# Kernel optimization log

Measured on AMD Instinct MI355X. Metric: run time of the kernel, lower is better.

## Reference

```python
import jax, jax.numpy as jnp
import numpy as np

TEMP = 1.0
POOL_K = 0.5
BN_EPS = 1e-5
B, N, D = 16, 256, 128


def setup_inputs() -> dict:
    key = jax.random.key(0)
    ks = jax.random.split(key, 8)
    s = 0.05
    return {
        "x": jax.random.normal(ks[0], (B, N, D), jnp.float32),
        "att_proj_w": jax.random.normal(ks[1], (D, D), jnp.float32) * s,
        "att_proj_b": jnp.zeros((D,), jnp.float32),
        "att_weight": jax.random.normal(ks[2], (D, 1), jnp.float32) * s,
        "pwa_w": jax.random.normal(ks[3], (D, D), jnp.float32) * s,
        "pwa_b": jnp.zeros((D,), jnp.float32),
        "pwoa_w": jax.random.normal(ks[4], (D, D), jnp.float32) * s,
        "pwoa_b": jnp.zeros((D,), jnp.float32),
        "bn_gamma": jnp.ones((D,), jnp.float32),
        "bn_beta": jnp.zeros((D,), jnp.float32),
        "bn_mean": jnp.zeros((D,), jnp.float32),
        "bn_var": jnp.ones((D,), jnp.float32),
        "pool_w": jax.random.normal(ks[5], (D, 1), jnp.float32) * s,
        "pool_b": jnp.zeros((1,), jnp.float32),
    }


def reference(x, att_proj_w, att_proj_b, att_weight, pwa_w, pwa_b,
              pwoa_w, pwoa_b, bn_gamma, bn_beta, bn_mean, bn_var,
              pool_w, pool_b):
    # ---- GraphAttentionLayer (eval mode: dropout = identity) ----
    # pairwise node outer product: (B, N, N, D)
    pair = x[:, :, None, :] * x[:, None, :, :]
    # att_proj + tanh, then project to scalar per node pair
    a = jnp.tanh(pair @ att_proj_w + att_proj_b)          # (B,N,N,D)
    logits = (a @ att_weight)[..., 0] / TEMP              # (B,N,N)
    # softmax over dim=-2 (the first node axis of the (N,N) map)
    att = jax.nn.softmax(logits, axis=1)                  # (B,N,N)
    # project: att_map @ x through proj_with_att, plus skip branch
    agg = jnp.einsum("bij,bjd->bid", att, x)              # (B,N,D)
    h = (agg @ pwa_w + pwa_b) + (x @ pwoa_w + pwoa_b)
    # BatchNorm1d in eval mode over feature dim
    h = (h - bn_mean) * jax.lax.rsqrt(bn_var + BN_EPS) * bn_gamma + bn_beta
    h = jax.nn.selu(h)
    # ---- GraphPool (eval mode: dropout = identity) ----
    scores = jax.nn.sigmoid(h @ pool_w + pool_b)          # (B,N,1)
    k_nodes = max(int(N * POOL_K), 1)
    _, idx = jax.lax.top_k(scores[..., 0], k_nodes)       # (B,k)
    hs = h * scores                                       # (B,N,D)
    out = jnp.take_along_axis(hs, idx[:, :, None], axis=1)  # (B,k,D)
    return out
```

## Files before the change

### kernel.cpp

```cpp
#include <hip/hip_runtime.h>
#include <math.h>

typedef float f32x4 __attribute__((ext_vector_type(4)));
typedef short s16x8 __attribute__((ext_vector_type(8)));

#define L2E 1.4426950408889634f
#define C2L2E 2.885390081777927f

__global__ void k0_prep(const float* __restrict__ W,
                        unsigned short* __restrict__ gWhi,
                        unsigned short* __restrict__ gWlo) {
  int t = blockIdx.x * 256 + threadIdx.x;
  int d = t >> 7, e = t & 127;
  float w = W[d * 128 + e];
  unsigned u = __float_as_uint(w);
  unsigned hb = (u + 0x7fffu + ((u >> 16) & 1u)) >> 16;
  float r = w - __uint_as_float(hb << 16);
  unsigned ul = __float_as_uint(r);
  unsigned lb = (ul + 0x7fffu + ((ul >> 16) & 1u)) >> 16;
  int addr = e * 128 + (d ^ ((e & 7) << 3));
  gWhi[addr] = (unsigned short)hb;
  gWlo[addr] = (unsigned short)lb;
}

__global__ __launch_bounds__(256, 2) void k1_logits(
    const float* __restrict__ x, const unsigned short* __restrict__ gWhi,
    const unsigned short* __restrict__ gWlo, const float* __restrict__ apb,
    const float* __restrict__ av, float* __restrict__ Lg) {
  __shared__ __align__(16) unsigned short sWhi[16384];
  __shared__ __align__(16) unsigned short sWlo[16384];
  __shared__ __align__(16) float sXj[16 * 132];

  int tt = blockIdx.x, ti = 0;
  while (tt >= 16 - ti) { tt -= 16 - ti; ++ti; }
  const int tj = ti + tt;
  const int b = blockIdx.y;
  const int i0 = ti * 16, j0 = tj * 16;
  const int tid = threadIdx.x;

  {
    const uint4* shi = (const uint4*)gWhi;
    const uint4* slo = (const uint4*)gWlo;
    uint4* dhi = (uint4*)sWhi;
    uint4* dlo = (uint4*)sWlo;
#pragma unroll
    for (int r = 0; r < 8; ++r) {
      dhi[tid + 256 * r] = shi[tid + 256 * r];
      dlo[tid + 256 * r] = slo[tid + 256 * r];
    }
    const float4* xsrc = (const float4*)(x + ((size_t)(b * 256 + j0)) * 128);
#pragma unroll
    for (int r = 0; r < 2; ++r) {
      int v = tid + 256 * r;
      *(float4*)&sXj[(v >> 5) * 132 + (v & 31) * 4] = xsrc[v];
    }
  }
  __syncthreads();

  const int lane = tid & 63;
  const int w = tid >> 6;
  const int quad = lane >> 4;
  const int col = lane & 15;
  const int swz = (col & 7) << 3;

  float vw[8];
  f32x4 acc[4][8];
#pragma unroll
  for (int et = 0; et < 8; ++et) {
    float bi = apb[col + 16 * et];
    vw[et] = av[col + 16 * et];
#pragma unroll
    for (int mt = 0; mt < 4; ++mt) acc[mt][et] = (f32x4){bi, bi, bi, bi};
  }

  const float* xib = x + ((size_t)(b * 256 + i0 + 4 * w)) * 128;

#pragma unroll
  for (int kstep = 0; kstep < 4; ++kstep) {
    const int k0 = kstep * 32 + quad * 8;
    float4 xj0 = *(const float4*)&sXj[col * 132 + k0];
    float4 xj1 = *(const float4*)&sXj[col * 132 + k0 + 4];
    s16x8 Ah[4], Al[4];
#pragma unroll
    for (int mt = 0; mt < 4; ++mt) {
      const float* xip = xib + mt * 128 + k0;
      float4 xi0 = *(const float4*)xip;
      float4 xi1 = *(const float4*)(xip + 4);
      float pv[8];
      pv[0] = xi0.x * xj0.x; pv[1] = xi0.y * xj0.y;
      pv[2] = xi0.z * xj0.z; pv[3] = xi0.w * xj0.w;
      pv[4] = xi1.x * xj1.x; pv[5] = xi1.y * xj1.y;
      pv[6] = xi1.z * xj1.z; pv[7] = xi1.w * xj1.w;
      uint4 hp, lp;
      unsigned* hq = (unsigned*)&hp;
      unsigned* lq = (unsigned*)&lp;
#pragma unroll
      for (int p = 0; p < 4; ++p) {
        unsigned u0 = __float_as_uint(pv[2 * p]);
        unsigned u1 = __float_as_uint(pv[2 * p + 1]);
        hq[p] = __builtin_amdgcn_perm(u1, u0, 0x07060302);
        float h0 = __uint_as_float(u0 & 0xffff0000u);
        float h1 = __uint_as_float(u1 & 0xffff0000u);
        unsigned v0 = __float_as_uint(pv[2 * p] - h0) + 0x8000u;
        unsigned v1 = __float_as_uint(pv[2 * p + 1] - h1) + 0x8000u;
        lq[p] = __builtin_amdgcn_perm(v1, v0, 0x07060302);
      }
      Ah[mt] = *(s16x8*)&hp;
      Al[mt] = *(s16x8*)&lp;
    }
#pragma unroll
    for (int et = 0; et < 8; ++et) {
      const int addr = (col + 16 * et) * 128 + (k0 ^ swz);
      s16x8 bh = *(const s16x8*)&sWhi[addr];
      s16x8 bl = *(const s16x8*)&sWlo[addr];
#pragma unroll
      for (int mt = 0; mt < 4; ++mt) {
        acc[mt][et] = __builtin_amdgcn_mfma_f32_16x16x32_bf16(Ah[mt], bh, acc[mt][et], 0, 0, 0);
        acc[mt][et] = __builtin_amdgcn_mfma_f32_16x16x32_bf16(Al[mt], bh, acc[mt][et], 0, 0, 0);
        acc[mt][et] = __builtin_amdgcn_mfma_f32_16x16x32_bf16(Ah[mt], bl, acc[mt][et], 0, 0, 0);
      }
    }
  }

  float fl[4];
#pragma unroll
  for (int mt = 0; mt < 4; ++mt) {
    float ls[4] = {0.f, 0.f, 0.f, 0.f};
#pragma unroll
    for (int et = 0; et < 8; ++et) {
#pragma unroll
      for (int r = 0; r < 4; ++r) {
        float e2 = __builtin_amdgcn_exp2f(acc[mt][et][r] * C2L2E);
        float t = 1.0f - 2.0f * __builtin_amdgcn_rcpf(e2 + 1.0f);
        ls[r] += t * vw[et];
      }
    }
#pragma unroll
    for (int m = 1; m < 16; m <<= 1) {
      ls[0] += __shfl_xor(ls[0], m);
      ls[1] += __shfl_xor(ls[1], m);
      ls[2] += __shfl_xor(ls[2], m);
      ls[3] += __shfl_xor(ls[3], m);
    }
    fl[mt] = (col == 0) ? ls[0] : (col == 1) ? ls[1] : (col == 2) ? ls[2] : ls[3];
  }
  if (col < 4) {
    const int j = j0 + quad * 4 + col;
    float4 val = {fl[0], fl[1], fl[2], fl[3]};
    *(float4*)&Lg[((size_t)(b * 256 + j)) * 256 + i0 + 4 * w] = val;
    if (ti != tj) {
#pragma unroll
      for (int mt = 0; mt < 4; ++mt)
        Lg[((size_t)(b * 256 + i0 + 4 * w + mt)) * 256 + j] = fl[mt];
    }
  }
}

__global__ void k2_softmax(float* __restrict__ Lg) {
  const int w = threadIdx.x >> 6, lane = threadIdx.x & 63;
  const int row = blockIdx.x * 4 + w;
  float4* p = (float4*)(Lg + (size_t)row * 256);
  float4 v = p[lane];
  float m = fmaxf(fmaxf(v.x, v.y), fmaxf(v.z, v.w));
#pragma unroll
  for (int mask = 1; mask < 64; mask <<= 1) m = fmaxf(m, __shfl_xor(m, mask));
  v.x = __builtin_amdgcn_exp2f((v.x - m) * L2E);
  v.y = __builtin_amdgcn_exp2f((v.y - m) * L2E);
  v.z = __builtin_amdgcn_exp2f((v.z - m) * L2E);
  v.w = __builtin_amdgcn_exp2f((v.w - m) * L2E);
  float s = v.x + v.y + v.z + v.w;
#pragma unroll
  for (int mask = 1; mask < 64; mask <<= 1) s += __shfl_xor(s, mask);
  float inv = 1.0f / s;
  v.x *= inv; v.y *= inv; v.z *= inv; v.w *= inv;
  p[lane] = v;
}

__global__ void k34_aggh(const float* __restrict__ Lg, const float* __restrict__ x,
                         const float* __restrict__ pwa, const float* __restrict__ pwoa,
                         const float* __restrict__ pwab, const float* __restrict__ pwob,
                         const float* __restrict__ gam, const float* __restrict__ bet,
                         const float* __restrict__ mea, const float* __restrict__ varr,
                         float* __restrict__ h) {
  const int b = blockIdx.y, i0 = blockIdx.x * 8;
  const int tid = threadIdx.x;
  const int il = tid >> 5, dl = tid & 31;
  __shared__ float satt[16][8];
  __shared__ float sxj[2048];
  __shared__ float sa[1024];
  __shared__ float sxi[1024];

  ((float4*)sxi)[tid] = ((const float4*)(x + ((size_t)(b * 256 + i0)) * 128))[tid];

  float acc[4] = {0.f, 0.f, 0.f, 0.f};
  for (int jj = 0; jj < 256; jj += 16) {
    __syncthreads();
    if (tid < 128)
      satt[tid >> 3][tid & 7] =
          Lg[((size_t)(b * 256 + jj + (tid >> 3))) * 256 + i0 + (tid & 7)];
    const float4* xsrc = (const float4*)(x + ((size_t)(b * 256 + jj)) * 128);
    ((float4*)sxj)[tid] = xsrc[tid];
    ((float4*)sxj)[tid + 256] = xsrc[tid + 256];
    __syncthreads();
#pragma unroll
    for (int jl = 0; jl < 16; ++jl) {
      float a = satt[jl][il];
      float4 xv = *(const float4*)&sxj[jl * 128 + dl * 4];
      acc[0] += a * xv.x; acc[1] += a * xv.y;
      acc[2] += a * xv.z; acc[3] += a * xv.w;
    }
  }
  __syncthreads();
  *(float4*)&sa[il * 128 + dl * 4] = *(float4*)acc;
  __syncthreads();

  double z[4] = {0, 0, 0, 0};
  for (int k = 0; k < 128; ++k) {
    double a = (double)sa[il * 128 + k];
    float4 wv = *(const float4*)(pwa + k * 128 + dl * 4);
    z[0] += a * (double)wv.x; z[1] += a * (double)wv.y;
    z[2] += a * (double)wv.z; z[3] += a * (double)wv.w;
  }
  for (int k = 0; k < 128; ++k) {
    double a = (double)sxi[il * 128 + k];
    float4 wv = *(const float4*)(pwoa + k * 128 + dl * 4);
    z[0] += a * (double)wv.x; z[1] += a * (double)wv.y;
    z[2] += a * (double)wv.z; z[3] += a * (double)wv.w;
  }
  float* dst = h + ((size_t)(b * 256 + i0 + il)) * 128 + dl * 4;
  float o[4];
#pragma unroll
  for (int q = 0; q < 4; ++q) {
    int d = dl * 4 + q;
    double hv = z[q] + (double)pwab[d] + (double)pwob[d];
    double bn = (hv - (double)mea[d]) * (1.0 / sqrt((double)varr[d] + 1e-5)) *
                    (double)gam[d] +
                (double)bet[d];
    float bf = (float)bn;
    o[q] = bf > 0.f ? 1.0507009873554805f * bf
                    : 1.7580993408473766f *
                          (__builtin_amdgcn_exp2f(bf * L2E) - 1.0f);
  }
  *(float4*)dst = *(float4*)o;
}

__global__ __launch_bounds__(1024) void k5_topk(const float* __restrict__ h,
                                                const float* __restrict__ plw,
                                                const float* __restrict__ plb,
                                                float* __restrict__ out) {
  const int b = blockIdx.x, tid = threadIdx.x;
  const int t = tid >> 2, c = tid & 3;
  __shared__ double part[256][4];
  __shared__ int ipart[256][4];
  __shared__ float sc[256];
  __shared__ int sel[128];

  {
    const float* hr = h + ((size_t)(b * 256 + t)) * 128 + c * 32;
    const float* wr = plw + c * 32;
    double z = 0.0;
    for (int k = 0; k < 32; ++k) z += (double)hr[k] * (double)wr[k];
    part[t][c] = z;
  }
  __syncthreads();
  if (c == 0) {
    double zz = part[t][0] + part[t][1] + part[t][2] + part[t][3] + (double)plb[0];
    sc[t] = (float)(1.0 / (1.0 + exp(-zz)));
  }
  __syncthreads();
  {
    const float st = sc[t];
    int r = 0;
    for (int m = c * 64; m < c * 64 + 64; ++m) {
      float sm = sc[m];
      r += (sm > st) || (sm == st && m < t);
    }
    ipart[t][c] = r;
  }
  __syncthreads();
  if (c == 0) {
    int rank = ipart[t][0] + ipart[t][1] + ipart[t][2] + ipart[t][3];
    if (rank < 128) sel[rank] = t;
  }
  __syncthreads();
  const float4* h4 = (const float4*)(h + (size_t)b * 256 * 128);
  float4* o4 = (float4*)(out + (size_t)b * 128 * 128);
#pragma unroll
  for (int r = 0; r < 4; ++r) {
    int v = tid + 1024 * r;
    int row = v >> 5, q = v & 31;
    int src = sel[row];
    float ss = sc[src];
    float4 hv = h4[src * 32 + q];
    float4 ov;
    ov.x = hv.x * ss; ov.y = hv.y * ss; ov.z = hv.z * ss; ov.w = hv.w * ss;
    o4[row * 32 + q] = ov;
  }
}

extern "C" void kernel_launch(void* const* d_in, const int* in_sizes, int n_in,
                              void* d_out, int out_size, void* d_ws, size_t ws_size,
                              hipStream_t stream) {
  const float* x    = (const float*)d_in[0];
  const float* apw  = (const float*)d_in[1];
  const float* apb  = (const float*)d_in[2];
  const float* av   = (const float*)d_in[3];
  const float* pwa  = (const float*)d_in[4];
  const float* pwab = (const float*)d_in[5];
  const float* pwoa = (const float*)d_in[6];
  const float* pwob = (const float*)d_in[7];
  const float* gam  = (const float*)d_in[8];
  const float* bet  = (const float*)d_in[9];
  const float* mea  = (const float*)d_in[10];
  const float* varr = (const float*)d_in[11];
  const float* plw  = (const float*)d_in[12];
  const float* plb  = (const float*)d_in[13];
  float* out = (float*)d_out;

  unsigned short* gWhi = (unsigned short*)d_ws;
  unsigned short* gWlo = gWhi + 16384;
  float* Lg = (float*)((char*)d_ws + 65536);
  float* hb = Lg + (size_t)16 * 256 * 256;

  k0_prep<<<64, 256, 0, stream>>>(apw, gWhi, gWlo);
  k1_logits<<<dim3(136, 16), 256, 0, stream>>>(x, gWhi, gWlo, apb, av, Lg);
  k2_softmax<<<1024, 256, 0, stream>>>(Lg);
  k34_aggh<<<dim3(32, 16), 256, 0, stream>>>(Lg, x, pwa, pwoa, pwab, pwob, gam,
                                             bet, mea, varr, hb);
  k5_topk<<<16, 1024, 0, stream>>>(hb, plw, plb, out);
}
```

Before: 189.2 us.

## Fuse softmax into logits kernel via exp and atomic row sums; move pool scores

```diff
diff --git a/kernel.cpp b/kernel.cpp
--- a/kernel.cpp
+++ b/kernel.cpp
@@ -9,27 +9,36 @@
 
 __global__ void k0_prep(const float* __restrict__ W,
                         unsigned short* __restrict__ gWhi,
-                        unsigned short* __restrict__ gWlo) {
-  int t = blockIdx.x * 256 + threadIdx.x;
-  int d = t >> 7, e = t & 127;
-  float w = W[d * 128 + e];
-  unsigned u = __float_as_uint(w);
-  unsigned hb = (u + 0x7fffu + ((u >> 16) & 1u)) >> 16;
-  float r = w - __uint_as_float(hb << 16);
-  unsigned ul = __float_as_uint(r);
-  unsigned lb = (ul + 0x7fffu + ((ul >> 16) & 1u)) >> 16;
-  int addr = e * 128 + (d ^ ((e & 7) << 3));
-  gWhi[addr] = (unsigned short)hb;
-  gWlo[addr] = (unsigned short)lb;
-}
-
-__global__ __launch_bounds__(256, 2) void k1_logits(
+                        unsigned short* __restrict__ gWlo,
+                        float* __restrict__ S) {
+  int bid = blockIdx.x;
+  if (bid < 64) {
+    int t = bid * 256 + threadIdx.x;
+    int d = t >> 7, e = t & 127;
+    float w = W[d * 128 + e];
+    unsigned u = __float_as_uint(w);
+    unsigned hb = (u + 0x7fffu + ((u >> 16) & 1u)) >> 16;
+    float r = w - __uint_as_float(hb << 16);
+    unsigned ul = __float_as_uint(r);
+    unsigned lb = (ul + 0x7fffu + ((ul >> 16) & 1u)) >> 16;
+    int addr = e * 128 + (d ^ ((e & 7) << 3));
+    gWhi[addr] = (unsigned short)hb;
+    gWlo[addr] = (unsigned short)lb;
+  } else {
+    S[(bid - 64) * 256 + threadIdx.x] = 0.f;
+  }
+}
+
+__global__ __launch_bounds__(256, 2) void kA_logits(
     const float* __restrict__ x, const unsigned short* __restrict__ gWhi,
     const unsigned short* __restrict__ gWlo, const float* __restrict__ apb,
-    const float* __restrict__ av, float* __restrict__ Lg) {
+    const float* __restrict__ av, float* __restrict__ Lg,
+    float* __restrict__ S) {
   __shared__ __align__(16) unsigned short sWhi[16384];
   __shared__ __align__(16) unsigned short sWlo[16384];
   __shared__ __align__(16) float sXj[16 * 132];
+  __shared__ float sRow[16][4];
+  __shared__ float sMir[16];
 
   int tt = blockIdx.x, ti = 0;
   while (tt >= 16 - ti) { tt -= 16 - ti; ++ti; }
@@ -122,7 +131,7 @@
     }
   }
 
-  float fl[4];
+  float E[4];
 #pragma unroll
   for (int mt = 0; mt < 4; ++mt) {
     float ls[4] = {0.f, 0.f, 0.f, 0.f};
@@ -142,54 +151,59 @@
       ls[2] += __shfl_xor(ls[2], m);
       ls[3] += __shfl_xor(ls[3], m);
     }
-    fl[mt] = (col == 0) ? ls[0] : (col == 1) ? ls[1] : (col == 2) ? ls[2] : ls[3];
-  }
+    float fl = (col == 0) ? ls[0] : (col == 1) ? ls[1] : (col == 2) ? ls[2] : ls[3];
+    E[mt] = __builtin_amdgcn_exp2f(fl * L2E);
+  }
+
   if (col < 4) {
     const int j = j0 + quad * 4 + col;
-    float4 val = {fl[0], fl[1], fl[2], fl[3]};
+    float4 val = {E[0], E[1], E[2], E[3]};
     *(float4*)&Lg[((size_t)(b * 256 + j)) * 256 + i0 + 4 * w] = val;
-    if (ti != tj) {
+    sRow[quad * 4 + col][w] = E[0] + E[1] + E[2] + E[3];
+  }
+
+  if (ti != tj) {
+    if (col < 4) {
+      const int j = j0 + quad * 4 + col;
 #pragma unroll
       for (int mt = 0; mt < 4; ++mt)
-        Lg[((size_t)(b * 256 + i0 + 4 * w + mt)) * 256 + j] = fl[mt];
-    }
-  }
-}
-
-__global__ void k2_softmax(float* __restrict__ Lg) {
-  const int w = threadIdx.x >> 6, lane = threadIdx.x & 63;
-  const int row = blockIdx.x * 4 + w;
-  float4* p = (float4*)(Lg + (size_t)row * 256);
-  float4 v = p[lane];
-  float m = fmaxf(fmaxf(v.x, v.y), fmaxf(v.z, v.w));
-#pragma unroll
-  for (int mask = 1; mask < 64; mask <<= 1) m = fmaxf(m, __shfl_xor(m, mask));
-  v.x = __builtin_amdgcn_exp2f((v.x - m) * L2E);
-  v.y = __builtin_amdgcn_exp2f((v.y - m) * L2E);
-  v.z = __builtin_amdgcn_exp2f((v.z - m) * L2E);
-  v.w = __builtin_amdgcn_exp2f((v.w - m) * L2E);
-  float s = v.x + v.y + v.z + v.w;
-#pragma unroll
-  for (int mask = 1; mask < 64; mask <<= 1) s += __shfl_xor(s, mask);
-  float inv = 1.0f / s;
-  v.x *= inv; v.y *= inv; v.z *= inv; v.w *= inv;
-  p[lane] = v;
-}
-
-__global__ void k34_aggh(const float* __restrict__ Lg, const float* __restrict__ x,
-                         const float* __restrict__ pwa, const float* __restrict__ pwoa,
-                         const float* __restrict__ pwab, const float* __restrict__ pwob,
-                         const float* __restrict__ gam, const float* __restrict__ bet,
-                         const float* __restrict__ mea, const float* __restrict__ varr,
-                         float* __restrict__ h) {
+        Lg[((size_t)(b * 256 + i0 + 4 * w + mt)) * 256 + j] = E[mt];
+    }
+#pragma unroll
+    for (int mt = 0; mt < 4; ++mt) {
+      float v = (col < 4) ? E[mt] : 0.f;
+#pragma unroll
+      for (int m = 1; m < 64; m <<= 1) v += __shfl_xor(v, m);
+      if (lane == 0) sMir[4 * w + mt] = v;
+    }
+  }
+  __syncthreads();
+  if (tid < 16) {
+    atomicAdd(&S[b * 256 + j0 + tid],
+              sRow[tid][0] + sRow[tid][1] + sRow[tid][2] + sRow[tid][3]);
+    if (ti != tj) atomicAdd(&S[b * 256 + i0 + tid], sMir[tid]);
+  }
+}
+
+__global__ void kB_aggh(const float* __restrict__ Lg, const float* __restrict__ S,
+                        const float* __restrict__ x,
+                        const float* __restrict__ pwa, const float* __restrict__ pwoa,
+                        const float* __restrict__ pwab, const float* __restrict__ pwob,
+                        const float* __restrict__ gam, const float* __restrict__ bet,
+                        const float* __restrict__ mea, const float* __restrict__ varr,
+                        const float* __restrict__ plw, const float* __restrict__ plb,
+                        float* __restrict__ h, float* __restrict__ scores) {
   const int b = blockIdx.y, i0 = blockIdx.x * 8;
   const int tid = threadIdx.x;
   const int il = tid >> 5, dl = tid & 31;
+  __shared__ float sInv[256];
   __shared__ float satt[16][8];
   __shared__ float sxj[2048];
   __shared__ float sa[1024];
   __shared__ float sxi[1024];
-
+  __shared__ double sScD[8][32];
+
+  sInv[tid] = 1.0f / S[b * 256 + tid];
   ((float4*)sxi)[tid] = ((const float4*)(x + ((size_t)(b * 256 + i0)) * 128))[tid];
 
   float acc[4] = {0.f, 0.f, 0.f, 0.f};
@@ -197,7 +211,8 @@
     __syncthreads();
     if (tid < 128)
       satt[tid >> 3][tid & 7] =
-          Lg[((size_t)(b * 256 + jj + (tid >> 3))) * 256 + i0 + (tid & 7)];
+          Lg[((size_t)(b * 256 + jj + (tid >> 3))) * 256 + i0 + (tid & 7)] *
+          sInv[jj + (tid >> 3)];
     const float4* xsrc = (const float4*)(x + ((size_t)(b * 256 + jj)) * 128);
     ((float4*)sxj)[tid] = xsrc[tid];
     ((float4*)sxj)[tid + 256] = xsrc[tid + 256];
@@ -227,7 +242,6 @@
     z[0] += a * (double)wv.x; z[1] += a * (double)wv.y;
     z[2] += a * (double)wv.z; z[3] += a * (double)wv.w;
   }
-  float* dst = h + ((size_t)(b * 256 + i0 + il)) * 128 + dl * 4;
   float o[4];
 #pragma unroll
   for (int q = 0; q < 4; ++q) {
@@ -241,32 +255,30 @@
                     : 1.7580993408473766f *
                           (__builtin_amdgcn_exp2f(bf * L2E) - 1.0f);
   }
-  *(float4*)dst = *(float4*)o;
-}
-
-__global__ __launch_bounds__(1024) void k5_topk(const float* __restrict__ h,
-                                                const float* __restrict__ plw,
-                                                const float* __restrict__ plb,
+  *(float4*)(h + ((size_t)(b * 256 + i0 + il)) * 128 + dl * 4) = *(float4*)o;
+
+  sScD[il][dl] = (double)o[0] * (double)plw[dl * 4] +
+                 (double)o[1] * (double)plw[dl * 4 + 1] +
+                 (double)o[2] * (double)plw[dl * 4 + 2] +
+                 (double)o[3] * (double)plw[dl * 4 + 3];
+  __syncthreads();
+  if (tid < 8) {
+    double zz = (double)plb[0];
+    for (int c = 0; c < 32; ++c) zz += sScD[tid][c];
+    scores[b * 256 + i0 + tid] = (float)(1.0 / (1.0 + exp(-zz)));
+  }
+}
+
+__global__ __launch_bounds__(1024) void kC_topk(const float* __restrict__ h,
+                                                const float* __restrict__ scores,
                                                 float* __restrict__ out) {
   const int b = blockIdx.x, tid = threadIdx.x;
   const int t = tid >> 2, c = tid & 3;
-  __shared__ double part[256][4];
+  __shared__ float sc[256];
   __shared__ int ipart[256][4];
-  __shared__ float sc[256];
   __shared__ int sel[128];
 
-  {
-    const float* hr = h + ((size_t)(b * 256 + t)) * 128 + c * 32;
-    const float* wr = plw + c * 32;
-    double z = 0.0;
-    for (int k = 0; k < 32; ++k) z += (double)hr[k] * (double)wr[k];
-    part[t][c] = z;
-  }
-  __syncthreads();
-  if (c == 0) {
-    double zz = part[t][0] + part[t][1] + part[t][2] + part[t][3] + (double)plb[0];
-    sc[t] = (float)(1.0 / (1.0 + exp(-zz)));
-  }
+  if (c == 0) sc[t] = scores[b * 256 + t];
   __syncthreads();
   {
     const float st = sc[t];
@@ -319,13 +331,14 @@
 
   unsigned short* gWhi = (unsigned short*)d_ws;
   unsigned short* gWlo = gWhi + 16384;
-  float* Lg = (float*)((char*)d_ws + 65536);
+  float* S  = (float*)((char*)d_ws + 65536);
+  float* Lg = (float*)((char*)d_ws + 81920);
   float* hb = Lg + (size_t)16 * 256 * 256;
-
-  k0_prep<<<64, 256, 0, stream>>>(apw, gWhi, gWlo);
-  k1_logits<<<dim3(136, 16), 256, 0, stream>>>(x, gWhi, gWlo, apb, av, Lg);
-  k2_softmax<<<1024, 256, 0, stream>>>(Lg);
-  k34_aggh<<<dim3(32, 16), 256, 0, stream>>>(Lg, x, pwa, pwoa, pwab, pwob, gam,
-                                             bet, mea, varr, hb);
-  k5_topk<<<16, 1024, 0, stream>>>(hb, plw, plb, out);
-}
+  float* sco = hb + (size_t)16 * 256 * 128;
+
+  k0_prep<<<80, 256, 0, stream>>>(apw, gWhi, gWlo, S);
+  kA_logits<<<dim3(136, 16), 256, 0, stream>>>(x, gWhi, gWlo, apb, av, Lg, S);
+  kB_aggh<<<dim3(32, 16), 256, 0, stream>>>(Lg, S, x, pwa, pwoa, pwab, pwob,
+                                            gam, bet, mea, varr, plw, plb, hb, sco);
+  kC_topk<<<16, 1024, 0, stream>>>(hb, sco, out);
+}
```

New measurement: 185.1 us. 2.2% less time.
